# Kernel tuning notes

Hardware: AMD Instinct MI355X
Metric: run time of the kernel (lower is better)

Reference implementation:

```python
import jax, jax.numpy as jnp
import numpy as np

B, T, C, H = 4, 2048, 1024, 16
D = C // H  # head_dim = 64


def setup_inputs() -> dict:
    key = jax.random.key(0)
    ks = jax.random.split(key, 5)
    scale = 0.02
    return {
        "x": jax.random.normal(ks[0], (B, T, C), dtype=jnp.float32),
        "w_qkv": jax.random.normal(ks[1], (C, 3 * C), dtype=jnp.float32) * scale,
        "b_qkv": jnp.zeros((3 * C,), dtype=jnp.float32),
        "w_out": jax.random.normal(ks[2], (C, C), dtype=jnp.float32) * scale,
        "b_out": jnp.zeros((C,), dtype=jnp.float32),
    }


def reference(x, w_qkv, b_qkv, w_out, b_out):
    Bx, Tx, Cx = x.shape
    qkv = x @ w_qkv + b_qkv  # [B,T,3C]
    q, k, v = jnp.split(qkv, 3, axis=-1)
    # [B,T,C] -> [B,H,T,D]
    def heads(t):
        return t.reshape(Bx, Tx, H, D).transpose(0, 2, 1, 3)
    q, k, v = heads(q), heads(k), heads(v)
    scores = jnp.einsum("bhtd,bhsd->bhts", q, k) / jnp.sqrt(jnp.float32(D))
    causal = jnp.tril(jnp.ones((Tx, Tx), dtype=bool))
    scores = jnp.where(causal[None, None], scores, -jnp.inf)
    attn = jax.nn.softmax(scores, axis=-1)
    y = jnp.einsum("bhts,bhsd->bhtd", attn, v)  # [B,H,T,D]
    y = y.transpose(0, 2, 1, 3).reshape(Bx, Tx, Cx)
    return y @ w_out + b_out
```

## Files before the change

kernel.cpp:

```cpp
#include <hip/hip_runtime.h>
#include <hip/hip_bf16.h>
#include <math.h>

typedef __bf16 bf16;
typedef __bf16 bf16x8 __attribute__((ext_vector_type(8)));
typedef __bf16 bf16x4 __attribute__((ext_vector_type(4)));
typedef __bf16 bf16x2 __attribute__((ext_vector_type(2)));
typedef float  f32x4  __attribute__((ext_vector_type(4)));

__device__ __forceinline__ void gld_lds16(const bf16* g, bf16* l) {
    void* gv = (void*)g;
    __builtin_amdgcn_global_load_lds(
        (__attribute__((address_space(1))) void*)gv,
        (__attribute__((address_space(3))) void*)l, 16, 0, 0);
}

__global__ void k_cvt_bf16(const float* __restrict__ in, bf16* __restrict__ out, int n4) {
    int i = blockIdx.x * blockDim.x + threadIdx.x;
    if (i < n4) {
        float4 v = ((const float4*)in)[i];
        bf16x4 o;
        o[0] = (bf16)v.x; o[1] = (bf16)v.y; o[2] = (bf16)v.z; o[3] = (bf16)v.w;
        ((bf16x4*)out)[i] = o;
    }
}

__global__ void k_transpose_cvt(const float* __restrict__ in, bf16* __restrict__ out,
                                int R, int C) {
    __shared__ float tile[64][68];
    int c0 = blockIdx.x * 64, r0 = blockIdx.y * 64;
    int tid = threadIdx.x;
#pragma unroll
    for (int i = 0; i < 4; ++i) {
        int chunk = tid + i * 256;
        int r = chunk >> 4, c4 = (chunk & 15) * 4;
        float4 v = *(const float4*)(in + (size_t)(r0 + r) * C + c0 + c4);
        tile[r][c4 + 0] = v.x; tile[r][c4 + 1] = v.y;
        tile[r][c4 + 2] = v.z; tile[r][c4 + 3] = v.w;
    }
    __syncthreads();
#pragma unroll
    for (int i = 0; i < 2; ++i) {
        int chunk = tid + i * 256;
        int c = chunk >> 3, k8 = (chunk & 7) * 8;
        bf16x8 v;
#pragma unroll
        for (int j = 0; j < 8; ++j) v[j] = (bf16)tile[k8 + j][c];
        *(bf16x8*)(out + (size_t)(c0 + c) * R + r0 + k8) = v;
    }
}

__global__ void k_transpose_v(const bf16* __restrict__ qkv, bf16* __restrict__ vt) {
    __shared__ bf16 tile[64][72];
    int bh = blockIdx.y, b = bh >> 4, h = bh & 15;
    int t0 = blockIdx.x * 64;
    int tid = threadIdx.x;
    const bf16* src = qkv + (size_t)(b * 2048 + t0) * 3072 + 2048 + h * 64;
#pragma unroll
    for (int i = 0; i < 2; ++i) {
        int chunk = tid + i * 256;
        int t = chunk >> 3, d8 = (chunk & 7) * 8;
        bf16x8 v = *(const bf16x8*)(src + (size_t)t * 3072 + d8);
#pragma unroll
        for (int j = 0; j < 8; ++j) tile[t][d8 + j] = v[j];
    }
    __syncthreads();
#pragma unroll
    for (int i = 0; i < 2; ++i) {
        int chunk = tid + i * 256;
        int d = chunk >> 3, t8 = (chunk & 7) * 8;
        bf16x8 v;
#pragma unroll
        for (int j = 0; j < 8; ++j) v[j] = tile[t8 + j][d];
        *(bf16x8*)(vt + ((size_t)bh * 64 + d) * 2048 + t0 + t8) = v;
    }
}

template <bool OUT_BF16>
__global__ __launch_bounds__(256, 2) void k_gemm(
    const bf16* __restrict__ A, const bf16* __restrict__ Bt,
    const float* __restrict__ bias, void* __restrict__ Cout,
    int M, int N, int K) {
    __shared__ __align__(16) bf16 lA[2][4096];
    __shared__ __align__(16) bf16 lB[2][4096];
    int tid = threadIdx.x;
    int wid = tid >> 6, lane = tid & 63;
    int quad = lane >> 4, l16 = lane & 15;
    int bm = blockIdx.y * 128, bn = blockIdx.x * 128;
    int wm = (wid >> 1) * 64, wn = (wid & 1) * 64;

    f32x4 zero = {0.f, 0.f, 0.f, 0.f};
    f32x4 acc[4][4];
#pragma unroll
    for (int i = 0; i < 4; ++i)
#pragma unroll
        for (int j = 0; j < 4; ++j) acc[i][j] = zero;

    for (int k0 = 0; k0 < K; k0 += 64) {
        __syncthreads();
#pragma unroll
        for (int i = 0; i < 4; ++i) {
            int j = (wid * 4 + i) * 64 + lane;
            int kf = j >> 9, row = (j & 511) >> 2, c8 = (j & 3) * 8;
            gld_lds16(A  + (size_t)(bm + row) * K + k0 + kf * 32 + c8, &lA[0][0] + (wid * 4 + i) * 512);
            gld_lds16(Bt + (size_t)(bn + row) * K + k0 + kf * 32 + c8, &lB[0][0] + (wid * 4 + i) * 512);
        }
        __syncthreads();
#pragma unroll
        for (int kk = 0; kk < 2; ++kk) {
            bf16x8 af[4], bg[4];
#pragma unroll
            for (int i = 0; i < 4; ++i) {
                af[i] = *(const bf16x8*)(&lA[kk][(wm + i * 16 + l16) * 32 + quad * 8]);
                bg[i] = *(const bf16x8*)(&lB[kk][(wn + i * 16 + l16) * 32 + quad * 8]);
            }
#pragma unroll
            for (int i = 0; i < 4; ++i)
#pragma unroll
                for (int j = 0; j < 4; ++j)
                    acc[i][j] = __builtin_amdgcn_mfma_f32_16x16x32_bf16(af[i], bg[j], acc[i][j], 0, 0, 0);
        }
    }
#pragma unroll
    for (int i = 0; i < 4; ++i) {
#pragma unroll
        for (int j = 0; j < 4; ++j) {
            int col = bn + wn + j * 16 + l16;
            float bv = bias ? bias[col] : 0.f;
#pragma unroll
            for (int r = 0; r < 4; ++r) {
                int row = bm + wm + i * 16 + quad * 4 + r;
                float v = acc[i][j][r] + bv;
                if (OUT_BF16) ((bf16*)Cout)[(size_t)row * N + col] = (bf16)v;
                else          ((float*)Cout)[(size_t)row * N + col] = v;
            }
        }
    }
}

__global__ __launch_bounds__(256, 3) void k_attn(
    const bf16* __restrict__ qkv,
    const bf16* __restrict__ vt,
    bf16* __restrict__ y) {
    __shared__ __align__(16) bf16 lK[2][4096];
    __shared__ __align__(16) bf16 lV[2][4096];
    __shared__ __align__(16) bf16 lP[4][32 * 72];

    const int T = 2048, CQ = 3072;
    int tid = threadIdx.x, wid = tid >> 6, lane = tid & 63;
    int quad = lane >> 4, l16 = lane & 15;
    int x = blockIdx.x;
    int bh = ((x & 7) << 3) | ((x >> 3) & 7);
    int qb = 15 - (x >> 6);
    int b = bh >> 4, h = bh & 15;
    int q0 = qb * 128;
    int rb = qb * 4 + wid;
    int mdiag = rb >> 1;
    int ntiles = qb * 2 + 2;

    const bf16* qbase = qkv + (size_t)(b * T + q0 + wid * 32) * CQ + h * 64;
    const bf16* kbase = qkv + (size_t)(b * T) * CQ + 1024 + h * 64;
    const bf16* vbase = vt + (size_t)bh * 64 * T;
    bf16* lPw = lP[wid];

    auto stage = [&](int kt, int buf) {
        int t0 = kt * 64;
#pragma unroll
        for (int i = 0; i < 2; ++i) {
            int j = (wid * 2 + i) * 64 + lane;
            int r = j >> 3;
            int cs = ((j ^ r) & 7) * 8;
            gld_lds16(kbase + (size_t)(t0 + r) * CQ + cs, &lK[buf][(wid * 2 + i) * 512]);
            gld_lds16(vbase + (size_t)r * T + t0 + cs,    &lV[buf][(wid * 2 + i) * 512]);
        }
    };

    const float QSCALE = 0.125f * 1.44269504088896341f;
    bf16x8 qf[2][2];
#pragma unroll
    for (int qi = 0; qi < 2; ++qi)
#pragma unroll
        for (int kf = 0; kf < 2; ++kf) {
            bf16x8 v = *(const bf16x8*)(qbase + (size_t)(qi * 16 + l16) * CQ + kf * 32 + quad * 8);
#pragma unroll
            for (int j = 0; j < 8; ++j) v[j] = (bf16)((float)v[j] * QSCALE);
            qf[qi][kf] = v;
        }

    f32x4 zero = {0.f, 0.f, 0.f, 0.f};
    f32x4 minit = {-14.4269504089f, -14.4269504089f, -14.4269504089f, -14.4269504089f};
    f32x4 o[2][4];
    f32x4 ls[2];
#pragma unroll
    for (int qi = 0; qi < 2; ++qi) {
        ls[qi] = zero;
#pragma unroll
        for (int i = 0; i < 4; ++i) o[qi][i] = zero;
    }
    bf16x8 ones;
#pragma unroll
    for (int j = 0; j < 8; ++j) ones[j] = (bf16)1.0f;

    stage(0, 0);
    for (int kt = 0; kt < ntiles; ++kt) {
        __syncthreads();
        if (kt + 1 < ntiles) stage(kt + 1, (kt + 1) & 1);
        if (kt > mdiag) continue;
        const bf16* Kb = lK[kt & 1];
        const bf16* Vb = lV[kt & 1];
        bool diag = (kt == mdiag);
        bool half = diag && !(rb & 1);
        int in_hi = half ? 2 : 4;

        f32x4 s[2][4];
#pragma unroll
        for (int qi = 0; qi < 2; ++qi)
#pragma unroll
            for (int in = 0; in < 4; ++in) s[qi][in] = minit;
#pragma unroll
        for (int kf = 0; kf < 2; ++kf)
            for (int in = 0; in < in_hi; ++in) {
                bf16x8 kb = *(const bf16x8*)(Kb + (in * 16 + l16) * 64 + (((kf * 4 + quad) ^ (l16 & 7)) * 8));
#pragma unroll
                for (int qi = 0; qi < 2; ++qi)
                    s[qi][in] = __builtin_amdgcn_mfma_f32_16x16x32_bf16(kb, qf[qi][kf], s[qi][in], 0, 0, 0);
            }

        bf16x8 vb[2][4];
#pragma unroll
        for (int kf = 0; kf < 2; ++kf)
#pragma unroll
            for (int dn = 0; dn < 4; ++dn)
                vb[kf][dn] = *(const bf16x8*)(Vb + (dn * 16 + l16) * 64 + (((kf * 4 + quad) ^ (l16 & 7)) * 8));

        int rl0 = (rb * 32) - kt * 64;
        for (int qi = 0; qi < 2; ++qi) {
            int qloc = rl0 + qi * 16 + l16;
#pragma unroll
            for (int in = 0; in < 4; ++in) {
                bf16x4 pk4;
                if (in >= in_hi) {
                    pk4[0] = pk4[1] = pk4[2] = pk4[3] = (bf16)0.f;
                } else {
#pragma unroll
                    for (int r = 0; r < 4; ++r) {
                        float e = __builtin_amdgcn_exp2f(s[qi][in][r]);
                        if (diag) {
                            int tloc = in * 16 + quad * 4 + r;
                            if (tloc > qloc) e = 0.f;
                        }
                        pk4[r] = (bf16)e;
                    }
                }
                *(bf16x4*)(lPw + (qi * 16 + l16) * 72 + in * 16 + quad * 4) = pk4;
            }
        }

#pragma unroll
        for (int qi = 0; qi < 2; ++qi)
#pragma unroll
            for (int kf = 0; kf < 2; ++kf) {
                bf16x8 pa = *(const bf16x8*)(lPw + (qi * 16 + l16) * 72 + kf * 32 + quad * 8);
                ls[qi] = __builtin_amdgcn_mfma_f32_16x16x32_bf16(pa, ones, ls[qi], 0, 0, 0);
#pragma unroll
                for (int dn = 0; dn < 4; ++dn)
                    o[qi][dn] = __builtin_amdgcn_mfma_f32_16x16x32_bf16(pa, vb[kf][dn], o[qi][dn], 0, 0, 0);
            }
    }

#pragma unroll
    for (int qi = 0; qi < 2; ++qi)
#pragma unroll
        for (int r = 0; r < 4; ++r) {
            float li = 1.f / ls[qi][r];
            int row = q0 + wid * 32 + qi * 16 + quad * 4 + r;
#pragma unroll
            for (int dn = 0; dn < 4; ++dn) {
                float v = o[qi][dn][r] * li;
                y[(size_t)(b * T + row) * 1024 + h * 64 + dn * 16 + l16] = (bf16)v;
            }
        }
}

extern "C" void kernel_launch(void* const* d_in, const int* in_sizes, int n_in,
                              void* d_out, int out_size, void* d_ws, size_t ws_size,
                              hipStream_t stream) {
    const float* x     = (const float*)d_in[0];
    const float* w_qkv = (const float*)d_in[1];
    const float* b_qkv = (const float*)d_in[2];
    const float* w_out = (const float*)d_in[3];
    const float* b_out = (const float*)d_in[4];
    float* out = (float*)d_out;

    const int B = 4, T = 2048, C = 1024, H = 16;
    const int M = B * T;

    char* ws = (char*)d_ws;
    bf16* xb    = (bf16*)(ws);
    bf16* wqkvT = (bf16*)(ws + (16ull << 20));
    bf16* woutT = (bf16*)(ws + (22ull << 20));
    bf16* qkvb  = (bf16*)(ws + (24ull << 20));
    bf16* yb    = (bf16*)(ws + (72ull << 20));
    bf16* vtb   = xb;

    k_cvt_bf16<<<(M * C / 4 + 255) / 256, 256, 0, stream>>>(x, xb, M * C / 4);
    k_transpose_cvt<<<dim3(3 * C / 64, C / 64), 256, 0, stream>>>(w_qkv, wqkvT, C, 3 * C);
    k_transpose_cvt<<<dim3(C / 64, C / 64), 256, 0, stream>>>(w_out, woutT, C, C);
    k_gemm<true><<<dim3(3 * C / 128, M / 128), 256, 0, stream>>>(xb, wqkvT, b_qkv, qkvb, M, 3 * C, C);
    k_transpose_v<<<dim3(T / 64, B * H), 256, 0, stream>>>(qkvb, vtb);
    k_attn<<<dim3(1024, 1), 256, 0, stream>>>(qkvb, vtb, yb);
    k_gemm<false><<<dim3(C / 128, M / 128), 256, 0, stream>>>(yb, woutT, b_out, out, M, C, C);
}
```

Before: 288.7 us.

## Load K/V fragments directly from global memory instead of LDS double-buffering

Result: slower. 352.2 us (+22.0%).

```diff
diff --git a/kernel.cpp b/kernel.cpp
--- a/kernel.cpp
+++ b/kernel.cpp
@@ -5,7 +5,6 @@
 typedef __bf16 bf16;
 typedef __bf16 bf16x8 __attribute__((ext_vector_type(8)));
 typedef __bf16 bf16x4 __attribute__((ext_vector_type(4)));
-typedef __bf16 bf16x2 __attribute__((ext_vector_type(2)));
 typedef float  f32x4  __attribute__((ext_vector_type(4)));
 
 __device__ __forceinline__ void gld_lds16(const bf16* g, bf16* l) {
@@ -138,12 +137,10 @@
     }
 }
 
-__global__ __launch_bounds__(256, 3) void k_attn(
+__global__ __launch_bounds__(256, 4) void k_attn(
     const bf16* __restrict__ qkv,
     const bf16* __restrict__ vt,
     bf16* __restrict__ y) {
-    __shared__ __align__(16) bf16 lK[2][4096];
-    __shared__ __align__(16) bf16 lV[2][4096];
     __shared__ __align__(16) bf16 lP[4][32 * 72];
 
     const int T = 2048, CQ = 3072;
@@ -156,24 +153,11 @@
     int q0 = qb * 128;
     int rb = qb * 4 + wid;
     int mdiag = rb >> 1;
-    int ntiles = qb * 2 + 2;
 
     const bf16* qbase = qkv + (size_t)(b * T + q0 + wid * 32) * CQ + h * 64;
-    const bf16* kbase = qkv + (size_t)(b * T) * CQ + 1024 + h * 64;
-    const bf16* vbase = vt + (size_t)bh * 64 * T;
+    const bf16* kbase = qkv + (size_t)(b * T + l16) * CQ + 1024 + h * 64 + quad * 8;
+    const bf16* vbase = vt + ((size_t)(bh * 64 + l16)) * T + quad * 8;
     bf16* lPw = lP[wid];
-
-    auto stage = [&](int kt, int buf) {
-        int t0 = kt * 64;
-#pragma unroll
-        for (int i = 0; i < 2; ++i) {
-            int j = (wid * 2 + i) * 64 + lane;
-            int r = j >> 3;
-            int cs = ((j ^ r) & 7) * 8;
-            gld_lds16(kbase + (size_t)(t0 + r) * CQ + cs, &lK[buf][(wid * 2 + i) * 512]);
-            gld_lds16(vbase + (size_t)r * T + t0 + cs,    &lV[buf][(wid * 2 + i) * 512]);
-        }
-    };
 
     const float QSCALE = 0.125f * 1.44269504088896341f;
     bf16x8 qf[2][2];
@@ -201,16 +185,10 @@
 #pragma unroll
     for (int j = 0; j < 8; ++j) ones[j] = (bf16)1.0f;
 
-    stage(0, 0);
-    for (int kt = 0; kt < ntiles; ++kt) {
-        __syncthreads();
-        if (kt + 1 < ntiles) stage(kt + 1, (kt + 1) & 1);
-        if (kt > mdiag) continue;
-        const bf16* Kb = lK[kt & 1];
-        const bf16* Vb = lV[kt & 1];
+    for (int kt = 0; kt <= mdiag; ++kt) {
+        const bf16* Kt = kbase + (size_t)kt * 64 * CQ;
+        const bf16* Vt = vbase + kt * 64;
         bool diag = (kt == mdiag);
-        bool half = diag && !(rb & 1);
-        int in_hi = half ? 2 : 4;
 
         f32x4 s[2][4];
 #pragma unroll
@@ -218,54 +196,60 @@
 #pragma unroll
             for (int in = 0; in < 4; ++in) s[qi][in] = minit;
 #pragma unroll
-        for (int kf = 0; kf < 2; ++kf)
-            for (int in = 0; in < in_hi; ++in) {
-                bf16x8 kb = *(const bf16x8*)(Kb + (in * 16 + l16) * 64 + (((kf * 4 + quad) ^ (l16 & 7)) * 8));
-#pragma unroll
-                for (int qi = 0; qi < 2; ++qi)
-                    s[qi][in] = __builtin_amdgcn_mfma_f32_16x16x32_bf16(kb, qf[qi][kf], s[qi][in], 0, 0, 0);
-            }
-
-        bf16x8 vb[2][4];
-#pragma unroll
-        for (int kf = 0; kf < 2; ++kf)
-#pragma unroll
-            for (int dn = 0; dn < 4; ++dn)
-                vb[kf][dn] = *(const bf16x8*)(Vb + (dn * 16 + l16) * 64 + (((kf * 4 + quad) ^ (l16 & 7)) * 8));
+        for (int in = 0; in < 4; ++in) {
+            bf16x8 kb0 = *(const bf16x8*)(Kt + (size_t)in * 16 * CQ);
+            bf16x8 kb1 = *(const bf16x8*)(Kt + (size_t)in * 16 * CQ + 32);
+            s[0][in] = __builtin_amdgcn_mfma_f32_16x16x32_bf16(kb0, qf[0][0], s[0][in], 0, 0, 0);
+            s[1][in] = __builtin_amdgcn_mfma_f32_16x16x32_bf16(kb0, qf[1][0], s[1][in], 0, 0, 0);
+            s[0][in] = __builtin_amdgcn_mfma_f32_16x16x32_bf16(kb1, qf[0][1], s[0][in], 0, 0, 0);
+            s[1][in] = __builtin_amdgcn_mfma_f32_16x16x32_bf16(kb1, qf[1][1], s[1][in], 0, 0, 0);
+        }
+
+        bf16x8 vb0[4];
+#pragma unroll
+        for (int dn = 0; dn < 4; ++dn)
+            vb0[dn] = *(const bf16x8*)(Vt + (size_t)dn * 16 * T);
 
         int rl0 = (rb * 32) - kt * 64;
+#pragma unroll
         for (int qi = 0; qi < 2; ++qi) {
             int qloc = rl0 + qi * 16 + l16;
 #pragma unroll
             for (int in = 0; in < 4; ++in) {
                 bf16x4 pk4;
-                if (in >= in_hi) {
-                    pk4[0] = pk4[1] = pk4[2] = pk4[3] = (bf16)0.f;
-                } else {
-#pragma unroll
-                    for (int r = 0; r < 4; ++r) {
-                        float e = __builtin_amdgcn_exp2f(s[qi][in][r]);
-                        if (diag) {
-                            int tloc = in * 16 + quad * 4 + r;
-                            if (tloc > qloc) e = 0.f;
-                        }
-                        pk4[r] = (bf16)e;
+#pragma unroll
+                for (int r = 0; r < 4; ++r) {
+                    float e = __builtin_amdgcn_exp2f(s[qi][in][r]);
+                    if (diag) {
+                        int tloc = in * 16 + quad * 4 + r;
+                        if (tloc > qloc) e = 0.f;
                     }
+                    pk4[r] = (bf16)e;
                 }
                 *(bf16x4*)(lPw + (qi * 16 + l16) * 72 + in * 16 + quad * 4) = pk4;
             }
         }
 
-#pragma unroll
-        for (int qi = 0; qi < 2; ++qi)
-#pragma unroll
-            for (int kf = 0; kf < 2; ++kf) {
-                bf16x8 pa = *(const bf16x8*)(lPw + (qi * 16 + l16) * 72 + kf * 32 + quad * 8);
-                ls[qi] = __builtin_amdgcn_mfma_f32_16x16x32_bf16(pa, ones, ls[qi], 0, 0, 0);
-#pragma unroll
-                for (int dn = 0; dn < 4; ++dn)
-                    o[qi][dn] = __builtin_amdgcn_mfma_f32_16x16x32_bf16(pa, vb[kf][dn], o[qi][dn], 0, 0, 0);
-            }
+        bf16x8 vb1[4];
+#pragma unroll
+        for (int dn = 0; dn < 4; ++dn)
+            vb1[dn] = *(const bf16x8*)(Vt + (size_t)dn * 16 * T + 32);
+
+        __builtin_amdgcn_s_setprio(1);
+#pragma unroll
+        for (int qi = 0; qi < 2; ++qi) {
+            bf16x8 pa0 = *(const bf16x8*)(lPw + (qi * 16 + l16) * 72 + quad * 8);
+            ls[qi] = __builtin_amdgcn_mfma_f32_16x16x32_bf16(pa0, ones, ls[qi], 0, 0, 0);
+#pragma unroll
+            for (int dn = 0; dn < 4; ++dn)
+                o[qi][dn] = __builtin_amdgcn_mfma_f32_16x16x32_bf16(pa0, vb0[dn], o[qi][dn], 0, 0, 0);
+            bf16x8 pa1 = *(const bf16x8*)(lPw + (qi * 16 + l16) * 72 + 32 + quad * 8);
+            ls[qi] = __builtin_amdgcn_mfma_f32_16x16x32_bf16(pa1, ones, ls[qi], 0, 0, 0);
+#pragma unroll
+            for (int dn = 0; dn < 4; ++dn)
+                o[qi][dn] = __builtin_amdgcn_mfma_f32_16x16x32_bf16(pa1, vb1[dn], o[qi][dn], 0, 0, 0);
+        }
+        __builtin_amdgcn_s_setprio(0);
     }
 
 #pragma unroll
```
